# Performance work log

Measured on AMD Instinct MI355X. Metric: run time of the kernel, lower is better.

The kernel has to match this reference:

```python
import jax, jax.numpy as jnp
import numpy as np

NUM_HEADS = 16

def setup_inputs() -> dict:
    key = jax.random.key(0)
    ks = jax.random.split(key, 8)
    B, S, D = 2, 2048, 1024
    H = NUM_HEADS
    s = 0.02
    return {
        "x": jax.random.normal(ks[0], (B, S, D), jnp.float32),
        "Wqkv": jax.random.normal(ks[1], (D, 3 * D), jnp.float32) * s,
        "bqkv": jnp.zeros((3 * D,), jnp.float32),
        "Wo": jax.random.normal(ks[2], (D, D), jnp.float32) * s,
        "bo": jnp.zeros((D,), jnp.float32),
        "mobius_scale": jnp.full((H,), 0.1, jnp.float32),
        "W1": jax.random.normal(ks[3], (D, D // 2), jnp.float32) * s,
        "b1": jnp.zeros((D // 2,), jnp.float32),
        "W2": jax.random.normal(ks[4], (D // 2, H), jnp.float32) * s,
        "b2": jnp.zeros((H,), jnp.float32),
        "adaptive_weight": jnp.full((1,), 0.1, jnp.float32),
    }

def reference(x, Wqkv, bqkv, Wo, bo, mobius_scale, W1, b1, W2, b2, adaptive_weight):
    B, S, D = x.shape
    H = NUM_HEADS
    dh = D // H
    # --- adaptive gating MLP on pooled context ---
    context = jnp.mean(x, axis=1, keepdims=True)                      # (B,1,D)
    h = jax.nn.gelu(context @ W1 + b1, approximate=False)             # (B,1,D/2)
    adaptive_factors = jax.nn.sigmoid(h @ W2 + b2)                    # (B,1,H)
    # --- incidence attention with mobius term ---
    qkv = (x @ Wqkv + bqkv).reshape(B, S, 3, H, dh)
    q, k, v = qkv[:, :, 0], qkv[:, :, 1], qkv[:, :, 2]                # (B,S,H,dh)
    scores = jnp.einsum("bshd,bthd->bhst", q, k) / jnp.sqrt(jnp.float32(dh))
    # Mobius map of the raw scores, learnable per-head scale
    scores = scores + mobius_scale[None, :, None, None] * (scores / (1.0 + scores * scores))
    attn = jax.nn.softmax(scores, axis=-1)                            # (B,H,S,S)
    out = jnp.einsum("bhst,bthd->bshd", attn, v).reshape(B, S, D)
    base_output = out @ Wo + bo                                       # (B,S,D)
    # --- training-path elementwise rescale ---
    adjustment = jnp.mean(adaptive_factors, axis=-1, keepdims=True)   # (B,1,1)
    return base_output * (1.0 + adaptive_weight * adjustment)
```

## Files before the change

kernel.cpp:

```cpp
#include <hip/hip_runtime.h>
#include <hip/hip_bf16.h>
#include <stdint.h>

typedef unsigned short u16;
typedef unsigned int u32;
typedef __attribute__((ext_vector_type(8))) short short8;
typedef __attribute__((ext_vector_type(4))) float f32x4;
typedef __attribute__((ext_vector_type(2))) float f32x2;
typedef __attribute__((ext_vector_type(4))) unsigned short u16x4;
typedef __attribute__((ext_vector_type(2))) unsigned int u32x2;

#define DEVFN static __device__ __forceinline__


DEVFN u16 f2bf(float f) {
  u32 u = __float_as_uint(f);
  u = (u + 0x7FFFu + ((u >> 16) & 1u)) >> 16;
  return (u16)u;
}

DEVFN u32 cvtpk_bf16(float lo, float hi) {
  u32 r;
  asm("v_cvt_pk_bf16_f32 %0, %1, %2" : "=v"(r) : "v"(lo), "v"(hi));
  return r;
}

DEVFN void gll16(const void* g, void* l) {
  __builtin_amdgcn_global_load_lds((const __attribute__((address_space(1))) u32*)g,
                                   (__attribute__((address_space(3))) u32*)l, 16, 0, 0);
}

__global__ void ctx_cvt_kernel(const float* __restrict__ x, float* __restrict__ ctx,
                               u16* __restrict__ xbf) {
  int blk = blockIdx.x;
  int b = blk >> 7;
  int s0 = (blk & 127) * 16;
  int t = threadIdx.x;
  const float* xb = x + ((size_t)b * 2048 + s0) * 1024 + t * 4;
  u16* ob = xbf + ((size_t)b * 2048 + s0) * 1024 + t * 4;
  float4 sum = {0.f, 0.f, 0.f, 0.f};
#pragma unroll
  for (int s = 0; s < 16; ++s) {
    float4 v = *(const float4*)(xb + (size_t)s * 1024);
    sum.x += v.x;
    sum.y += v.y;
    sum.z += v.z;
    sum.w += v.w;
    u16x4 o = {f2bf(v.x), f2bf(v.y), f2bf(v.z), f2bf(v.w)};
    *(u16x4*)(ob + (size_t)s * 1024) = o;
  }
  float* c = ctx + b * 1024 + t * 4;
  atomicAdd(c + 0, sum.x);
  atomicAdd(c + 1, sum.y);
  atomicAdd(c + 2, sum.z);
  atomicAdd(c + 3, sum.w);
}

__global__ void adaptive1_kernel(const float* __restrict__ ctx, const float* __restrict__ W1,
                                 const float* __restrict__ b1, float* __restrict__ hbuf) {
  int b = blockIdx.x >> 4, jq = blockIdx.x & 15;
  int t = threadIdx.x;
  int jl = t & 31, dp = t >> 5;
  int j = jq * 32 + jl;
  __shared__ float ctxs[1024];
  __shared__ float partial[8][32];
  for (int i = t; i < 1024; i += 256) ctxs[i] = ctx[b * 1024 + i] * (1.0f / 2048.0f);
  __syncthreads();
  float a0 = 0.f, a1 = 0.f;
  int d0 = dp * 128;
  for (int d = d0; d < d0 + 128; d += 2) {
    a0 += ctxs[d] * W1[(size_t)d * 512 + j];
    a1 += ctxs[d + 1] * W1[(size_t)(d + 1) * 512 + j];
  }
  partial[dp][jl] = a0 + a1;
  __syncthreads();
  if (t < 32) {
    float acc = b1[jq * 32 + t];
#pragma unroll
    for (int p = 0; p < 8; ++p) acc += partial[p][t];
    hbuf[b * 512 + jq * 32 + t] =
        0.5f * acc * (1.0f + erff(acc * 0.70710678118654752f));
  }
}

__global__ void adaptive2_kernel(const float* __restrict__ hbuf, const float* __restrict__ W2,
                                 const float* __restrict__ b2, const float* __restrict__ aw,
                                 float* __restrict__ scale) {
  int b = blockIdx.x;
  int t = threadIdx.x;
  __shared__ float part[256];
  int o = t & 15, seg = t >> 4;
  float a = 0.f;
  for (int j = seg * 32; j < seg * 32 + 32; ++j) a += hbuf[b * 512 + j] * W2[(size_t)j * 16 + o];
  part[t] = a;
  __syncthreads();
  if (t < 16) {
    float acc = b2[t];
    for (int s2 = 0; s2 < 16; ++s2) acc += part[s2 * 16 + t];
    part[t] = 1.0f / (1.0f + __expf(-acc));
  }
  __syncthreads();
  if (t == 0) {
    float s = 0.f;
    for (int i = 0; i < 16; ++i) s += part[i];
    scale[b] = 1.0f + aw[0] * (s * (1.0f / 16.0f));
  }
}

__global__ void transpose_bf16_kernel(const float* __restrict__ in, u16* __restrict__ out,
                                      int K, int N) {
  __shared__ u16 tile[32][33];
  int n0 = blockIdx.x * 32, k0 = blockIdx.y * 32;
  int tc = threadIdx.x & 31, tr = threadIdx.x >> 5;
  for (int i = tr; i < 32; i += 8)
    tile[i][tc] = f2bf(in[(size_t)(k0 + i) * N + n0 + tc]);
  __syncthreads();
  for (int i = tr; i < 32; i += 8)
    out[(size_t)(n0 + i) * K + k0 + tc] = tile[tc][i];
}


DEVFN void gemm_tile_mainloop(const u16* __restrict__ A, const u16* __restrict__ Bt,
                              int m0, int n0, int K, u16* As, u16* Bs, f32x4 acc[4][4]) {
  const int tid = threadIdx.x;
  const int lane = tid & 63, wid = tid >> 6;
  const int wr = wid >> 1, wc = wid & 1;
  const int lr = lane & 15, lg = lane >> 4;
  const int srow = tid >> 2;
  const int scol = ((tid & 3) ^ ((tid >> 3) & 3)) * 8;
  const int axor = ((lr >> 1) & 3) << 4;

  const u16* ag0 = A + (size_t)(m0 + srow) * K + scol;
  const u16* ag1 = ag0 + (size_t)64 * K;
  const u16* bg0 = Bt + (size_t)(n0 + srow) * K + scol;
  const u16* bg1 = bg0 + (size_t)64 * K;

  gll16(ag0, As + tid * 8);
  gll16(ag1, As + (tid + 256) * 8);
  gll16(bg0, Bs + tid * 8);
  gll16(bg1, Bs + (tid + 256) * 8);

  int cur = 0;
  for (int k0 = 0; k0 < K; k0 += 32) {
    __syncthreads();
    if (k0 + 32 < K) {
      int nb = (cur ^ 1) * 4096;
      gll16(ag0 + k0 + 32, As + nb + tid * 8);
      gll16(ag1 + k0 + 32, As + nb + (tid + 256) * 8);
      gll16(bg0 + k0 + 32, Bs + nb + tid * 8);
      gll16(bg1 + k0 + 32, Bs + nb + (tid + 256) * 8);
    }
    const char* Ac = (const char*)(As + cur * 4096);
    const char* Bc = (const char*)(Bs + cur * 4096);
    short8 af[4], bf[4];
#pragma unroll
    for (int i = 0; i < 4; ++i)
      af[i] = *(const short8*)(Ac + (wr * 64 + i * 16 + lr) * 64 + ((lg * 16) ^ axor));
#pragma unroll
    for (int j = 0; j < 4; ++j)
      bf[j] = *(const short8*)(Bc + (wc * 64 + j * 16 + lr) * 64 + ((lg * 16) ^ axor));
#pragma unroll
    for (int i = 0; i < 4; ++i)
#pragma unroll
      for (int j = 0; j < 4; ++j)
        acc[i][j] = __builtin_amdgcn_mfma_f32_16x16x32_bf16(bf[j], af[i], acc[i][j], 0, 0, 0);
    cur ^= 1;
  }
}

DEVFN void gemm64_mainloop(const u16* __restrict__ A, const u16* __restrict__ Bt,
                           int m0, int n0, int K, u16* As, u16* Bs, f32x4 acc[2][2]) {
  const int tid = threadIdx.x;
  const int lane = tid & 63, wid = tid >> 6;
  const int wr = wid >> 1, wc = wid & 1;
  const int lr = lane & 15, lg = lane >> 4;
  const int srow = tid >> 2;
  const int scol = ((tid & 3) ^ ((tid >> 3) & 3)) * 8;
  const int axor = ((lr >> 1) & 3) << 4;

  const u16* ag = A + (size_t)(m0 + srow) * K + scol;
  const u16* bg = Bt + (size_t)(n0 + srow) * K + scol;
  gll16(ag, As + tid * 8);
  gll16(bg, Bs + tid * 8);

  int cur = 0;
  for (int k0 = 0; k0 < K; k0 += 32) {
    __syncthreads();
    if (k0 + 32 < K) {
      int nb = (cur ^ 1) * 2048;
      gll16(ag + k0 + 32, As + nb + tid * 8);
      gll16(bg + k0 + 32, Bs + nb + tid * 8);
    }
    const char* Ac = (const char*)(As + cur * 2048);
    const char* Bc = (const char*)(Bs + cur * 2048);
    short8 af[2], bf[2];
#pragma unroll
    for (int i = 0; i < 2; ++i)
      af[i] = *(const short8*)(Ac + (wr * 32 + i * 16 + lr) * 64 + ((lg * 16) ^ axor));
#pragma unroll
    for (int j = 0; j < 2; ++j)
      bf[j] = *(const short8*)(Bc + (wc * 32 + j * 16 + lr) * 64 + ((lg * 16) ^ axor));
#pragma unroll
    for (int i = 0; i < 2; ++i)
#pragma unroll
      for (int j = 0; j < 2; ++j)
        acc[i][j] = __builtin_amdgcn_mfma_f32_16x16x32_bf16(bf[j], af[i], acc[i][j], 0, 0, 0);
    cur ^= 1;
  }
}

__global__ __launch_bounds__(256) void gemm_qkv_kernel(
    const u16* __restrict__ A, const u16* __restrict__ Bt, const float* __restrict__ bias,
    u16* __restrict__ Qb, u16* __restrict__ Kb, u16* __restrict__ Vt) {
  __shared__ __align__(16) u16 As[2 * 128 * 32];
  __shared__ __align__(16) u16 Bs[2 * 128 * 32];
  f32x4 acc[4][4];
  const f32x4 z = {0.f, 0.f, 0.f, 0.f};
#pragma unroll
  for (int i = 0; i < 4; ++i)
#pragma unroll
    for (int j = 0; j < 4; ++j) acc[i][j] = z;
  int lin = blockIdx.x;
  int swz = (lin & 7) * 96 + (lin >> 3);
  int n0 = (swz % 24) * 128, m0 = (swz / 24) * 128;
  gemm_tile_mainloop(A, Bt, m0, n0, 1024, As, Bs, acc);

  const int lane = threadIdx.x & 63, wid = threadIdx.x >> 6;
  const int wr = wid >> 1, wc = wid & 1, lr = lane & 15, lg = lane >> 4;
#pragma unroll
  for (int i = 0; i < 4; ++i) {
    int m = m0 + wr * 64 + i * 16 + lr;
#pragma unroll
    for (int j = 0; j < 4; ++j) {
      int nb = n0 + wc * 64 + j * 16 + lg * 4;
      float4 bv = *(const float4*)&bias[nb];
      int c3 = nb >> 10;
      if (c3 == 2) {
        int bb = m >> 11, ss = m & 2047;
        int hh = (nb >> 6) & 15, dd = nb & 63;
        size_t vb_ = (((size_t)bb * 16 + hh) * 64 + dd) * 2048 + ss;
        Vt[vb_] = f2bf(acc[i][j][0] + bv.x);
        Vt[vb_ + 2048] = f2bf(acc[i][j][1] + bv.y);
        Vt[vb_ + 4096] = f2bf(acc[i][j][2] + bv.z);
        Vt[vb_ + 6144] = f2bf(acc[i][j][3] + bv.w);
      } else {
        u16* dst = (c3 == 0) ? Qb : Kb;
        float qs = (c3 == 0) ? 0.125f : 1.0f;
        u16x4 o = {f2bf((acc[i][j][0] + bv.x) * qs), f2bf((acc[i][j][1] + bv.y) * qs),
                   f2bf((acc[i][j][2] + bv.z) * qs), f2bf((acc[i][j][3] + bv.w) * qs)};
        *(u16x4*)&dst[(size_t)m * 1024 + (nb & 1023)] = o;
      }
    }
  }
}

__global__ __launch_bounds__(256) void gemm_out_kernel(
    const u16* __restrict__ A, const u16* __restrict__ Bt, const float* __restrict__ bo,
    const float* __restrict__ scale, float* __restrict__ out) {
  __shared__ __align__(16) u16 As[2 * 64 * 32];
  __shared__ __align__(16) u16 Bs[2 * 64 * 32];
  f32x4 acc[2][2];
  const f32x4 z = {0.f, 0.f, 0.f, 0.f};
#pragma unroll
  for (int i = 0; i < 2; ++i)
#pragma unroll
    for (int j = 0; j < 2; ++j) acc[i][j] = z;
  int lin = blockIdx.x;
  int swz = (lin & 7) * 128 + (lin >> 3);
  int n0 = (swz & 15) * 64, m0 = (swz >> 4) * 64;
  gemm64_mainloop(A, Bt, m0, n0, 1024, As, Bs, acc);

  const int lane = threadIdx.x & 63, wid = threadIdx.x >> 6;
  const int wr = wid >> 1, wc = wid & 1, lr = lane & 15, lg = lane >> 4;
#pragma unroll
  for (int i = 0; i < 2; ++i) {
    int m = m0 + wr * 32 + i * 16 + lr;
    float sc = scale[m >> 11];
#pragma unroll
    for (int j = 0; j < 2; ++j) {
      int nb = n0 + wc * 32 + j * 16 + lg * 4;
      float4 bv = *(const float4*)&bo[nb];
      float4 o = {(acc[i][j][0] + bv.x) * sc, (acc[i][j][1] + bv.y) * sc,
                  (acc[i][j][2] + bv.z) * sc, (acc[i][j][3] + bv.w) * sc};
      *(float4*)&out[(size_t)m * 1024 + nb] = o;
    }
  }
}

__global__ __launch_bounds__(512, 6) void attn_kernel(
    const u16* __restrict__ Qb, const u16* __restrict__ Kb, const u16* __restrict__ Vt,
    const float* __restrict__ mobius, u16* __restrict__ O) {
  __shared__ __align__(16) char smem[40960];
  u16* Ks = (u16*)smem;
  u16* Vs = (u16*)(smem + 16384);
  u16* Ps = (u16*)(smem + 32768);
  const int tid = threadIdx.x;
  const int lane = tid & 63, w = tid >> 6;
  const int qg = w >> 1, half = w & 1;
  const int lr = lane & 15, lg = lane >> 4;
  const int bid = blockIdx.x;
  const int bidx = (bid & 7) * 128 + (bid >> 3);
  const int qb = bidx & 31, h = (bidx >> 5) & 15, b = bidx >> 9;
  const float msc = mobius[h];

  const int srow = tid >> 3;
  const int scol = ((tid & 7) ^ (srow & 7)) * 8;
  const int rxor = (lr & 7) << 4;

  const u16* qgl = Qb + (size_t)(b * 2048 + qb * 64 + qg * 16 + lr) * 1024 + h * 64 + lg * 8;
  short8 qf0 = *(const short8*)qgl;
  short8 qf1 = *(const short8*)(qgl + 32);

  const u16* kg = Kb + (size_t)(b * 2048 + srow) * 1024 + h * 64 + scol;
  const u16* vg = Vt + ((size_t)(b * 16 + h) * 64 + srow) * 2048 + scol;

  gll16(kg, Ks + tid * 8);
  gll16(vg, Vs + tid * 8);

  float m_run = -3.0e38f, l_run = 0.0f;
  f32x4 acc_o[4];
  const f32x4 z = {0.f, 0.f, 0.f, 0.f};
#pragma unroll
  for (int i = 0; i < 4; ++i) acc_o[i] = z;

  const float L2E = 1.44269504f;
  const f32x2 one2 = {1.0f, 1.0f};
  const f32x2 msc2 = {msc, msc};
  const f32x2 l2e2 = {L2E, L2E};
  const int ki0 = half * 2;
  const int qrow = qg * 16 + lr;
  const char* Pc = (const char*)Ps;
  int cur = 0;
  for (int kt = 0; kt < 32; ++kt) {
    __syncthreads();
    if (kt < 31) {
      int nb = (cur ^ 1) * 4096;
      gll16(kg + (size_t)(kt + 1) * 64 * 1024, Ks + nb + tid * 8);
      gll16(vg + (kt + 1) * 64, Vs + nb + tid * 8);
    }
    const char* Kc = (const char*)(Ks + cur * 4096);
    const char* Vc = (const char*)(Vs + cur * 4096);

    f32x4 sacc[2];
#pragma unroll
    for (int i = 0; i < 2; ++i) sacc[i] = z;
    __builtin_amdgcn_s_setprio(1);
#pragma unroll
    for (int kk = 0; kk < 2; ++kk) {
      int krow = (ki0 + kk) * 16 + lr;
      short8 kfa = *(const short8*)(Kc + krow * 128 + ((lg * 16) ^ rxor));
      sacc[kk] = __builtin_amdgcn_mfma_f32_16x16x32_bf16(kfa, qf0, sacc[kk], 0, 0, 0);
      short8 kfb = *(const short8*)(Kc + krow * 128 + ((64 + lg * 16) ^ rxor));
      sacc[kk] = __builtin_amdgcn_mfma_f32_16x16x32_bf16(kfb, qf1, sacc[kk], 0, 0, 0);
    }
    __builtin_amdgcn_s_setprio(0);

    f32x2 p2[4];
    f32x2 mx = {-3.0e38f, -3.0e38f};
#pragma unroll
    for (int i = 0; i < 4; ++i) {
      int kk = i >> 1, jj = i & 1;
      f32x2 s = {sacc[kk][jj * 2], sacc[kk][jj * 2 + 1]};
      f32x2 d = s * s + one2;
      f32x2 rr = {__builtin_amdgcn_rcpf(d.x), __builtin_amdgcn_rcpf(d.y)};
      f32x2 tl = (msc2 * (s * rr) + s) * l2e2;
      p2[i] = tl;
      mx = __builtin_elementwise_max(mx, tl);
    }
    float tmax = fmaxf(mx.x, mx.y);
    tmax = fmaxf(tmax, __shfl_xor(tmax, 16));
    tmax = fmaxf(tmax, __shfl_xor(tmax, 32));
    if (__any(tmax > m_run + 8.0f)) {
      float m_new = fmaxf(m_run, tmax);
      float corr = __builtin_amdgcn_exp2f(m_run - m_new);
      m_run = m_new;
      l_run *= corr;
#pragma unroll
      for (int di = 0; di < 4; ++di)
#pragma unroll
        for (int r = 0; r < 4; ++r) acc_o[di][r] *= corr;
    }
    f32x2 m2 = {m_run, m_run};
    f32x2 sum2 = {0.f, 0.f};
#pragma unroll
    for (int i = 0; i < 4; ++i) {
      f32x2 e = p2[i] - m2;
      f32x2 pe = {__builtin_amdgcn_exp2f(e.x), __builtin_amdgcn_exp2f(e.y)};
      p2[i] = pe;
      sum2 += pe;
    }
    float tsum = sum2.x + sum2.y;
    tsum += __shfl_xor(tsum, 16);
    tsum += __shfl_xor(tsum, 32);
    l_run += tsum;

#pragma unroll
    for (int kk = 0; kk < 2; ++kk) {
      u32x2 pw = {cvtpk_bf16(p2[2 * kk].x, p2[2 * kk].y),
                  cvtpk_bf16(p2[2 * kk + 1].x, p2[2 * kk + 1].y)};
      *(u32x2*)(Pc + qrow * 128 + (((ki0 + kk) * 32 + lg * 8) ^ rxor)) = pw;
    }

    __builtin_amdgcn_s_setprio(1);
    {
      int cbx = (half * 64 + lg * 16) ^ rxor;
      short8 pf = *(const short8*)(Pc + qrow * 128 + cbx);
#pragma unroll
      for (int di = 0; di < 4; ++di) {
        short8 vf = *(const short8*)(Vc + (di * 16 + lr) * 128 + cbx);
        acc_o[di] = __builtin_amdgcn_mfma_f32_16x16x32_bf16(vf, pf, acc_o[di], 0, 0, 0);
      }
    }
    __builtin_amdgcn_s_setprio(0);
    cur ^= 1;
  }

  __syncthreads();
  float* xch = (float*)smem;
  if (half) {
    float* dst = xch + ((qg * 64) + lane) * 18;
#pragma unroll
    for (int di = 0; di < 4; ++di)
#pragma unroll
      for (int r = 0; r < 4; ++r) dst[di * 4 + r] = acc_o[di][r];
    dst[16] = m_run;
    dst[17] = l_run;
  }
  __syncthreads();
  if (!half) {
    const float* src = xch + ((qg * 64) + lane) * 18;
    float m1 = src[16], l1 = src[17];
    float m01 = fmaxf(m_run, m1);
    float a0 = __builtin_amdgcn_exp2f(m_run - m01);
    float a1 = __builtin_amdgcn_exp2f(m1 - m01);
    float linv = 1.0f / (l_run * a0 + l1 * a1);
    size_t obase = ((size_t)(b * 2048 + qb * 64 + qg * 16 + lr)) * 1024 + h * 64;
#pragma unroll
    for (int di = 0; di < 4; ++di) {
      float o0 = (acc_o[di][0] * a0 + src[di * 4 + 0] * a1) * linv;
      float o1 = (acc_o[di][1] * a0 + src[di * 4 + 1] * a1) * linv;
      float o2 = (acc_o[di][2] * a0 + src[di * 4 + 2] * a1) * linv;
      float o3 = (acc_o[di][3] * a0 + src[di * 4 + 3] * a1) * linv;
      u32x2 o = {cvtpk_bf16(o0, o1), cvtpk_bf16(o2, o3)};
      *(u32x2*)&O[obase + di * 16 + lg * 4] = o;
    }
  }
}


extern "C" void kernel_launch(void* const* d_in, const int* in_sizes, int n_in,
                              void* d_out, int out_size, void* d_ws, size_t ws_size,
                              hipStream_t stream) {
  const float* x = (const float*)d_in[0];
  const float* Wqkv = (const float*)d_in[1];
  const float* bqkv = (const float*)d_in[2];
  const float* Wo = (const float*)d_in[3];
  const float* bo = (const float*)d_in[4];
  const float* mob = (const float*)d_in[5];
  const float* W1 = (const float*)d_in[6];
  const float* b1 = (const float*)d_in[7];
  const float* W2 = (const float*)d_in[8];
  const float* b2 = (const float*)d_in[9];
  const float* aw = (const float*)d_in[10];
  float* out = (float*)d_out;

  const size_t MB = 1024 * 1024;
  char* ws = (char*)d_ws;
  float* scale = (float*)ws;
  float* ctx = (float*)(ws + 256);
  float* hbuf = (float*)(ws + 16384);
  char* base = ws + 32768;
  u16* xbf = (u16*)base;
  u16* wqkvT = (u16*)(base + 8 * MB);
  u16* woT = (u16*)(base + 14 * MB);
  u16* Qb = (u16*)(base + 16 * MB);
  u16* Kb = (u16*)(base + 24 * MB);
  u16* Vt = (u16*)(base + 32 * MB);
  u16* attn = (u16*)(base + 40 * MB);

  hipMemsetAsync(ctx, 0, 2048 * sizeof(float), stream);
  ctx_cvt_kernel<<<256, 256, 0, stream>>>(x, ctx, xbf);
  adaptive1_kernel<<<32, 256, 0, stream>>>(ctx, W1, b1, hbuf);
  adaptive2_kernel<<<2, 256, 0, stream>>>(hbuf, W2, b2, aw, scale);
  transpose_bf16_kernel<<<dim3(96, 32), 256, 0, stream>>>(Wqkv, wqkvT, 1024, 3072);
  transpose_bf16_kernel<<<dim3(32, 32), 256, 0, stream>>>(Wo, woT, 1024, 1024);
  gemm_qkv_kernel<<<768, 256, 0, stream>>>(xbf, wqkvT, bqkv, Qb, Kb, Vt);
  attn_kernel<<<1024, 512, 0, stream>>>(Qb, Kb, Vt, mob, attn);
  gemm_out_kernel<<<1024, 256, 0, stream>>>(attn, woT, bo, scale, out);
}
```

Measured before the change: 260.0 us.

## Widen adaptive MLP grid, merge weight transposes, use 128x128 tiles for out GEMM

Adaptive layer one now spreads work across 256 blocks of 4 outputs each, with a shared-memory tree reduction, so the 32-block launch no longer underuses the GPU. The two weight-transpose launches are merged into one kernel that picks its matrix from the block index, removing a launch. The output projection GEMM switches from 64x64 tiles (1024 blocks) to the 128x128 tile mainloop (256 blocks), improving data reuse per block. The catch is that 256 blocks may fill the CUs less evenly.

```diff
diff --git a/kernel.cpp b/kernel.cpp
--- a/kernel.cpp
+++ b/kernel.cpp
@@ -58,27 +58,30 @@
 
 __global__ void adaptive1_kernel(const float* __restrict__ ctx, const float* __restrict__ W1,
                                  const float* __restrict__ b1, float* __restrict__ hbuf) {
-  int b = blockIdx.x >> 4, jq = blockIdx.x & 15;
+  int b = blockIdx.x >> 7, jg = blockIdx.x & 127;
   int t = threadIdx.x;
-  int jl = t & 31, dp = t >> 5;
-  int j = jq * 32 + jl;
+  int jl = t & 3, dp = t >> 2;
+  int j = jg * 4 + jl;
   __shared__ float ctxs[1024];
-  __shared__ float partial[8][32];
+  __shared__ float partial[256];
   for (int i = t; i < 1024; i += 256) ctxs[i] = ctx[b * 1024 + i] * (1.0f / 2048.0f);
   __syncthreads();
   float a0 = 0.f, a1 = 0.f;
-  int d0 = dp * 128;
-  for (int d = d0; d < d0 + 128; d += 2) {
+  int d0 = dp * 16;
+#pragma unroll
+  for (int d = d0; d < d0 + 16; d += 2) {
     a0 += ctxs[d] * W1[(size_t)d * 512 + j];
     a1 += ctxs[d + 1] * W1[(size_t)(d + 1) * 512 + j];
   }
-  partial[dp][jl] = a0 + a1;
-  __syncthreads();
-  if (t < 32) {
-    float acc = b1[jq * 32 + t];
-#pragma unroll
-    for (int p = 0; p < 8; ++p) acc += partial[p][t];
-    hbuf[b * 512 + jq * 32 + t] =
+  partial[t] = a0 + a1;
+  __syncthreads();
+  for (int off = 128; off >= 4; off >>= 1) {
+    if (t < off) partial[t] += partial[t + off];
+    __syncthreads();
+  }
+  if (t < 4) {
+    float acc = b1[jg * 4 + t] + partial[t];
+    hbuf[b * 512 + jg * 4 + t] =
         0.5f * acc * (1.0f + erff(acc * 0.70710678118654752f));
   }
 }
@@ -107,16 +110,27 @@
   }
 }
 
-__global__ void transpose_bf16_kernel(const float* __restrict__ in, u16* __restrict__ out,
-                                      int K, int N) {
+__global__ void transpose_both_kernel(const float* __restrict__ Wqkv, u16* __restrict__ wqkvT,
+                                      const float* __restrict__ Wo, u16* __restrict__ woT) {
   __shared__ u16 tile[32][33];
-  int n0 = blockIdx.x * 32, k0 = blockIdx.y * 32;
+  int bid = blockIdx.x;
+  const float* in;
+  u16* out;
+  int N, n0, k0;
+  if (bid < 3072) {
+    in = Wqkv; out = wqkvT; N = 3072;
+    n0 = (bid % 96) * 32; k0 = (bid / 96) * 32;
+  } else {
+    bid -= 3072;
+    in = Wo; out = woT; N = 1024;
+    n0 = (bid & 31) * 32; k0 = (bid >> 5) * 32;
+  }
   int tc = threadIdx.x & 31, tr = threadIdx.x >> 5;
   for (int i = tr; i < 32; i += 8)
     tile[i][tc] = f2bf(in[(size_t)(k0 + i) * N + n0 + tc]);
   __syncthreads();
   for (int i = tr; i < 32; i += 8)
-    out[(size_t)(n0 + i) * K + k0 + tc] = tile[tc][i];
+    out[(size_t)(n0 + i) * 1024 + k0 + tc] = tile[tc][i];
 }
 
 
@@ -163,47 +177,6 @@
     for (int i = 0; i < 4; ++i)
 #pragma unroll
       for (int j = 0; j < 4; ++j)
-        acc[i][j] = __builtin_amdgcn_mfma_f32_16x16x32_bf16(bf[j], af[i], acc[i][j], 0, 0, 0);
-    cur ^= 1;
-  }
-}
-
-DEVFN void gemm64_mainloop(const u16* __restrict__ A, const u16* __restrict__ Bt,
-                           int m0, int n0, int K, u16* As, u16* Bs, f32x4 acc[2][2]) {
-  const int tid = threadIdx.x;
-  const int lane = tid & 63, wid = tid >> 6;
-  const int wr = wid >> 1, wc = wid & 1;
-  const int lr = lane & 15, lg = lane >> 4;
-  const int srow = tid >> 2;
-  const int scol = ((tid & 3) ^ ((tid >> 3) & 3)) * 8;
-  const int axor = ((lr >> 1) & 3) << 4;
-
-  const u16* ag = A + (size_t)(m0 + srow) * K + scol;
-  const u16* bg = Bt + (size_t)(n0 + srow) * K + scol;
-  gll16(ag, As + tid * 8);
-  gll16(bg, Bs + tid * 8);
-
-  int cur = 0;
-  for (int k0 = 0; k0 < K; k0 += 32) {
-    __syncthreads();
-    if (k0 + 32 < K) {
-      int nb = (cur ^ 1) * 2048;
-      gll16(ag + k0 + 32, As + nb + tid * 8);
-      gll16(bg + k0 + 32, Bs + nb + tid * 8);
-    }
-    const char* Ac = (const char*)(As + cur * 2048);
-    const char* Bc = (const char*)(Bs + cur * 2048);
-    short8 af[2], bf[2];
-#pragma unroll
-    for (int i = 0; i < 2; ++i)
-      af[i] = *(const short8*)(Ac + (wr * 32 + i * 16 + lr) * 64 + ((lg * 16) ^ axor));
-#pragma unroll
-    for (int j = 0; j < 2; ++j)
-      bf[j] = *(const short8*)(Bc + (wc * 32 + j * 16 + lr) * 64 + ((lg * 16) ^ axor));
-#pragma unroll
-    for (int i = 0; i < 2; ++i)
-#pragma unroll
-      for (int j = 0; j < 2; ++j)
         acc[i][j] = __builtin_amdgcn_mfma_f32_16x16x32_bf16(bf[j], af[i], acc[i][j], 0, 0, 0);
     cur ^= 1;
   }
@@ -257,28 +230,28 @@
 __global__ __launch_bounds__(256) void gemm_out_kernel(
     const u16* __restrict__ A, const u16* __restrict__ Bt, const float* __restrict__ bo,
     const float* __restrict__ scale, float* __restrict__ out) {
-  __shared__ __align__(16) u16 As[2 * 64 * 32];
-  __shared__ __align__(16) u16 Bs[2 * 64 * 32];
-  f32x4 acc[2][2];
+  __shared__ __align__(16) u16 As[2 * 128 * 32];
+  __shared__ __align__(16) u16 Bs[2 * 128 * 32];
+  f32x4 acc[4][4];
   const f32x4 z = {0.f, 0.f, 0.f, 0.f};
 #pragma unroll
-  for (int i = 0; i < 2; ++i)
-#pragma unroll
-    for (int j = 0; j < 2; ++j) acc[i][j] = z;
+  for (int i = 0; i < 4; ++i)
+#pragma unroll
+    for (int j = 0; j < 4; ++j) acc[i][j] = z;
   int lin = blockIdx.x;
-  int swz = (lin & 7) * 128 + (lin >> 3);
-  int n0 = (swz & 15) * 64, m0 = (swz >> 4) * 64;
-  gemm64_mainloop(A, Bt, m0, n0, 1024, As, Bs, acc);
+  int swz = (lin & 7) * 32 + (lin >> 3);
+  int n0 = (swz & 7) * 128, m0 = (swz >> 3) * 128;
+  gemm_tile_mainloop(A, Bt, m0, n0, 1024, As, Bs, acc);
 
   const int lane = threadIdx.x & 63, wid = threadIdx.x >> 6;
   const int wr = wid >> 1, wc = wid & 1, lr = lane & 15, lg = lane >> 4;
 #pragma unroll
-  for (int i = 0; i < 2; ++i) {
-    int m = m0 + wr * 32 + i * 16 + lr;
+  for (int i = 0; i < 4; ++i) {
+    int m = m0 + wr * 64 + i * 16 + lr;
     float sc = scale[m >> 11];
 #pragma unroll
-    for (int j = 0; j < 2; ++j) {
-      int nb = n0 + wc * 32 + j * 16 + lg * 4;
+    for (int j = 0; j < 4; ++j) {
+      int nb = n0 + wc * 64 + j * 16 + lg * 4;
       float4 bv = *(const float4*)&bo[nb];
       float4 o = {(acc[i][j][0] + bv.x) * sc, (acc[i][j][1] + bv.y) * sc,
                   (acc[i][j][2] + bv.z) * sc, (acc[i][j][3] + bv.w) * sc};
@@ -480,11 +453,10 @@
 
   hipMemsetAsync(ctx, 0, 2048 * sizeof(float), stream);
   ctx_cvt_kernel<<<256, 256, 0, stream>>>(x, ctx, xbf);
-  adaptive1_kernel<<<32, 256, 0, stream>>>(ctx, W1, b1, hbuf);
+  adaptive1_kernel<<<256, 256, 0, stream>>>(ctx, W1, b1, hbuf);
   adaptive2_kernel<<<2, 256, 0, stream>>>(hbuf, W2, b2, aw, scale);
-  transpose_bf16_kernel<<<dim3(96, 32), 256, 0, stream>>>(Wqkv, wqkvT, 1024, 3072);
-  transpose_bf16_kernel<<<dim3(32, 32), 256, 0, stream>>>(Wo, woT, 1024, 1024);
+  transpose_both_kernel<<<4096, 256, 0, stream>>>(Wqkv, wqkvT, Wo, woT);
   gemm_qkv_kernel<<<768, 256, 0, stream>>>(xbf, wqkvT, bqkv, Qb, Kb, Vt);
   attn_kernel<<<1024, 512, 0, stream>>>(Qb, Kb, Vt, mob, attn);
-  gemm_out_kernel<<<1024, 256, 0, stream>>>(attn, woT, bo, scale, out);
-}
+  gemm_out_kernel<<<256, 256, 0, stream>>>(attn, woT, bo, scale, out);
+}
```

Measured after the change: 257.0 us. About the same (-1.2%).
